# Optimization experiments

Measured on AMD Instinct MI355X. Metric: run time of the kernel, lower is better.

The kernel has to match this reference:

```python
import jax, jax.numpy as jnp
import numpy as np

HIDDEN = 4096
NUM_HEADS = 32
NUM_KV_HEADS = 8
HEAD_DIM = 128
T = 2048
ROPE_THETA = 10000.0


def setup_inputs() -> dict:
    key = jax.random.key(0)
    ks = jax.random.split(key, 10)
    s = 0.02
    return {
        "hidden_states": jax.random.normal(ks[0], (T, HIDDEN), dtype=jnp.float32),
        "positions": jnp.arange(T, dtype=jnp.int32),
        "Wq": jax.random.normal(ks[1], (NUM_HEADS * HEAD_DIM, HIDDEN), dtype=jnp.float32) * s,
        "bq": jax.random.normal(ks[2], (NUM_HEADS * HEAD_DIM,), dtype=jnp.float32) * s,
        "Wk": jax.random.normal(ks[3], (NUM_KV_HEADS * HEAD_DIM, HIDDEN), dtype=jnp.float32) * s,
        "bk": jax.random.normal(ks[4], (NUM_KV_HEADS * HEAD_DIM,), dtype=jnp.float32) * s,
        "Wv": jax.random.normal(ks[5], (NUM_KV_HEADS * HEAD_DIM, HIDDEN), dtype=jnp.float32) * s,
        "bv": jax.random.normal(ks[6], (NUM_KV_HEADS * HEAD_DIM,), dtype=jnp.float32) * s,
        "Wo": jax.random.normal(ks[7], (HIDDEN, HIDDEN), dtype=jnp.float32) * s,
        "bo": jax.random.normal(ks[8], (HIDDEN,), dtype=jnp.float32) * s,
    }


def _rope_cos_sin(positions, head_dim, base):
    # neox-style rotary over the full head_dim
    half = head_dim // 2
    inv_freq = 1.0 / (base ** (jnp.arange(0, half, dtype=jnp.float32) * 2.0 / head_dim))
    angles = positions.astype(jnp.float32)[:, None] * inv_freq[None, :]  # [T, half]
    return jnp.cos(angles), jnp.sin(angles)


def _apply_rope(x, cos, sin):
    # x: [T, H, D]; neox: split halves, rotate
    half = x.shape[-1] // 2
    x1, x2 = x[..., :half], x[..., half:]
    c = cos[:, None, :]
    s = sin[:, None, :]
    return jnp.concatenate([x1 * c - x2 * s, x2 * c + x1 * s], axis=-1)


def reference(hidden_states, positions, Wq, bq, Wk, bk, Wv, bv, Wo, bo):
    q = (hidden_states @ Wq.T + bq).reshape(T, NUM_HEADS, HEAD_DIM)
    k = (hidden_states @ Wk.T + bk).reshape(T, NUM_KV_HEADS, HEAD_DIM)
    v = (hidden_states @ Wv.T + bv).reshape(T, NUM_KV_HEADS, HEAD_DIM)

    cos, sin = _rope_cos_sin(positions, HEAD_DIM, ROPE_THETA)
    q = _apply_rope(q, cos, sin)
    k = _apply_rope(k, cos, sin)

    scale = 1.0 / np.sqrt(HEAD_DIM).astype(np.float32)
    group = NUM_HEADS // NUM_KV_HEADS
    qg = q.reshape(T, NUM_KV_HEADS, group, HEAD_DIM)
    # scores: [g_kv, r, q, k] without materializing repeated KV heads
    scores = jnp.einsum('qgrd,kgd->grqk', qg, k) * scale
    causal = positions[:, None] >= positions[None, :]  # [T, T]
    scores = jnp.where(causal[None, None], scores, jnp.finfo(scores.dtype).min)
    probs = jax.nn.softmax(scores, axis=-1)
    o = jnp.einsum('grqk,kgd->qgrd', probs, v).reshape(T, NUM_HEADS * HEAD_DIM)
    return o @ Wo.T + bo
```

## Files before the change

### kernel.cpp

```cpp
#include <hip/hip_runtime.h>
#include <stdint.h>

typedef unsigned short u16;
typedef __bf16 bf16x8_t __attribute__((ext_vector_type(8)));
typedef float f32x4_t __attribute__((ext_vector_type(4)));

#define T_SEQ 2048
#define HID 4096
#define ROWQKV 6144

__device__ __forceinline__ float bf2f(u16 x){ return __uint_as_float(((uint32_t)x)<<16); }
__device__ __forceinline__ u16 f2bf(float f){
  uint32_t u = __float_as_uint(f);
  return (u16)((u + 0x7fffu + ((u>>16)&1u)) >> 16);
}

__device__ __forceinline__ void gload16(const void* g, void* l){
  __builtin_amdgcn_global_load_lds(
      (const __attribute__((address_space(1))) uint32_t*)g,
      (__attribute__((address_space(3))) uint32_t*)l, 16, 0, 0);
}

__global__ void cvt_kernel(const float* __restrict__ src, u16* __restrict__ dst, int n8){
  int i = blockIdx.x*blockDim.x + threadIdx.x;
  if (i >= n8) return;
  const float4* s = (const float4*)src;
  float4 a = s[2*i], b = s[2*i+1];
  union { u16 u[8]; uint4 v; } o;
  o.u[0]=f2bf(a.x); o.u[1]=f2bf(a.y); o.u[2]=f2bf(a.z); o.u[3]=f2bf(a.w);
  o.u[4]=f2bf(b.x); o.u[5]=f2bf(b.y); o.u[6]=f2bf(b.z); o.u[7]=f2bf(b.w);
  ((uint4*)dst)[i] = o.v;
}

__global__ void setup_kernel(const float* __restrict__ bq, const float* __restrict__ bk,
                             const float* __restrict__ bv, const int* __restrict__ pos,
                             float* __restrict__ bqkv, float* __restrict__ cost,
                             float* __restrict__ sint){
  int i = blockIdx.x*blockDim.x + threadIdx.x;
  if (i < 6144) bqkv[i] = (i<4096) ? bq[i] : ((i<5120) ? bk[i-4096] : bv[i-5120]);
  if (i < T_SEQ*64){
    int t = i >> 6, d = i & 63;
    float inv = powf(10000.0f, -(float)(2*d) / 128.0f);
    float ang = (float)pos[t] * inv;
    cost[i] = cosf(ang);
    sint[i] = sinf(ang);
  }
}

#define BUF2 32768

#define GBAR __builtin_amdgcn_s_barrier()
#define LGKM0 do{ asm volatile("s_waitcnt lgkmcnt(0)" ::: "memory"); \
                  __builtin_amdgcn_sched_barrier(0); }while(0)

#define AREAD2(mh, ck) do{ \
  const u16* ab = &lds[cur + aoff + (mh)*4096]; \
  afr[0] = *(const bf16x8_t*)&ab[0*1024 + (ck)]; \
  afr[1] = *(const bf16x8_t*)&ab[1*1024 + (ck)]; \
  afr[2] = *(const bf16x8_t*)&ab[2*1024 + (ck)]; \
  afr[3] = *(const bf16x8_t*)&ab[3*1024 + (ck)]; }while(0)

#define BREAD2(ck) do{ \
  const u16* bb = &lds[cur + boff]; \
  bfr[0] = *(const bf16x8_t*)&bb[0*1024 + (ck)]; \
  bfr[1] = *(const bf16x8_t*)&bb[1*1024 + (ck)]; \
  bfr[2] = *(const bf16x8_t*)&bb[2*1024 + (ck)]; \
  bfr[3] = *(const bf16x8_t*)&bb[3*1024 + (ck)]; }while(0)

#define MM16(mh) do{ \
  _Pragma("unroll") \
  for (int mi=0; mi<4; ++mi){ \
    _Pragma("unroll") \
    for (int n=0; n<4; ++n) \
      acc[(mh)*4+mi][n] = __builtin_amdgcn_mfma_f32_16x16x32_bf16(afr[mi], bfr[n], acc[(mh)*4+mi][n],0,0,0); \
  } }while(0)

template<bool OUT_BF16>
__global__ __launch_bounds__(512, 2)
void gemm_t2(const u16* __restrict__ A, const u16* __restrict__ B,
             const float* __restrict__ bias, u16* __restrict__ Cb,
             float* __restrict__ Cf, int K, int N)
{
  __shared__ u16 lds[2*BUF2];
  const int tid = threadIdx.x, lane = tid & 63, w = tid >> 6;
  const int l15 = lane & 15, l4 = lane >> 4;
  const int wm = w >> 2, wn = w & 3;

  const int nwg = gridDim.x * gridDim.y;
  int flat = blockIdx.y * gridDim.x + blockIdx.x;
  flat = (flat & 7) * (nwg >> 3) + (flat >> 3);
  const int bx = flat % gridDim.x, by = flat / gridDim.x;
  const int bm = by * 256, bn = bx * 256;

  const int srow = w*8 + (lane >> 3);
  const int swc  = ((lane & 7) ^ (lane >> 3)) * 8;
  const u16* pAlo = A + (size_t)(bm +       srow)*K + swc;
  const u16* pAhi = A + (size_t)(bm + 128 + srow)*K + swc;
  const u16* pBlo = B + (size_t)(bn +       srow)*K + swc;
  const u16* pBhi = B + (size_t)(bn + 128 + srow)*K + swc;
  const size_t j64 = (size_t)64*K;
  const int wu = (w*8)*64;

  const int cA0 = ((0 + l4) ^ (l15 & 7)) * 8;
  const int cA1 = ((4 + l4) ^ (l15 & 7)) * 8;
  const int aoff = (wm*128 + l15) * 64;
  const int boff = 16384 + (wn*64 + l15) * 64;

  f32x4_t acc[8][4] = {};
  const int KT = K >> 6;

  gload16(pAlo,       &lds[0     + wu]);  gload16(pAlo + j64, &lds[4096  + wu]);
  gload16(pAhi,       &lds[8192  + wu]);  gload16(pAhi + j64, &lds[12288 + wu]);
  gload16(pBlo,       &lds[16384 + wu]);  gload16(pBlo + j64, &lds[20480 + wu]);
  gload16(pBhi,       &lds[24576 + wu]);  gload16(pBhi + j64, &lds[28672 + wu]);
  pAlo += 64; pAhi += 64; pBlo += 64; pBhi += 64;
  asm volatile("s_waitcnt vmcnt(0)" ::: "memory");
  GBAR;

  for (int t = 0; t < KT; ++t){
    const int cur = (t & 1) * BUF2;
    const int nxt = ((t + 1) & 1) * BUF2;
    const bool st = (t + 1 < KT);
    bf16x8_t afr[4], bfr[4];

    BREAD2(cA0); AREAD2(0, cA0);
    if (st){
      gload16(pAlo,       &lds[nxt + 0     + wu]);
      gload16(pAlo + j64, &lds[nxt + 4096  + wu]);
      gload16(pAhi,       &lds[nxt + 8192  + wu]);
      gload16(pAhi + j64, &lds[nxt + 12288 + wu]);
    }
    GBAR; LGKM0;
    __builtin_amdgcn_s_setprio(1); MM16(0); __builtin_amdgcn_s_setprio(0);
    GBAR;

    AREAD2(1, cA0);
    if (st){
      gload16(pBlo,       &lds[nxt + 16384 + wu]);
      gload16(pBlo + j64, &lds[nxt + 20480 + wu]);
      gload16(pBhi,       &lds[nxt + 24576 + wu]);
      gload16(pBhi + j64, &lds[nxt + 28672 + wu]);
      pAlo += 64; pAhi += 64; pBlo += 64; pBhi += 64;
    }
    GBAR; LGKM0;
    __builtin_amdgcn_s_setprio(1); MM16(1); __builtin_amdgcn_s_setprio(0);
    GBAR;

    BREAD2(cA1); AREAD2(0, cA1);
    GBAR; LGKM0;
    __builtin_amdgcn_s_setprio(1); MM16(0); __builtin_amdgcn_s_setprio(0);
    GBAR;

    AREAD2(1, cA1);
    GBAR; LGKM0;
    __builtin_amdgcn_s_setprio(1); MM16(1); __builtin_amdgcn_s_setprio(0);
    if (st) asm volatile("s_waitcnt vmcnt(0)" ::: "memory");
    GBAR;
  }

  #pragma unroll
  for (int m=0;m<8;m++){
    #pragma unroll
    for (int n=0;n<4;n++){
      #pragma unroll
      for (int j=0;j<4;j++){
        int row = bm + wm*128 + (m>>2)*64 + (m&3)*16 + l4*4 + j;
        int col = bn + wn*64 + n*16 + l15;
        float v = acc[m][n][j] + bias[col];
        if constexpr (OUT_BF16) Cb[(size_t)row*N + col] = f2bf(v);
        else                    Cf[(size_t)row*N + col] = v;
      }
    }
  }
}

__global__ void rope_kernel(u16* __restrict__ qkv, const float* __restrict__ cost,
                            const float* __restrict__ sint){
  int i = blockIdx.x*blockDim.x + threadIdx.x;
  int t = i / 2560;
  int r = i % 2560;
  int h = r >> 6, d = r & 63;
  int base = (h < 32) ? h*128 : (4096 + (h-32)*128);
  size_t p1 = (size_t)t*ROWQKV + base + d;
  float x1 = bf2f(qkv[p1]), x2 = bf2f(qkv[p1+64]);
  float c = cost[(t<<6)+d], s = sint[(t<<6)+d];
  qkv[p1]    = f2bf(x1*c - x2*s);
  qkv[p1+64] = f2bf(x2*c + x1*s);
}

#define KLD 136
#define VLD 72
#define PLD 72

__global__ __launch_bounds__(256)
void attn_kernel(const u16* __restrict__ qkv, u16* __restrict__ attn_o)
{
  __shared__ u16 Ks[64*KLD];
  __shared__ u16 Vt[128*VLD];
  __shared__ u16 Ps[64*PLD];
  const int tid = threadIdx.x, lane = tid&63, wid = tid>>6;
  const int l15 = lane&15, l4 = lane>>4;
  const int h  = blockIdx.x & 31;
  const int qt = 31 - (blockIdx.x >> 5);
  const int q0 = qt * 64;
  const int kvh = h >> 2;
  const u16* Qg = qkv + h*128;
  const u16* Kg = qkv + 4096 + kvh*128;
  const u16* Vg = qkv + 5120 + kvh*128;

  bf16x8_t qf[4];
  {
    size_t qrow = (size_t)(q0 + wid*16 + l15);
    #pragma unroll
    for (int kk=0;kk<4;kk++)
      qf[kk] = *(const bf16x8_t*)(Qg + qrow*ROWQKV + kk*32 + l4*8);
  }
  float mrow[4] = {-1e30f,-1e30f,-1e30f,-1e30f};
  float lrow[4] = {0.f,0.f,0.f,0.f};
  f32x4_t oacc[8] = {};
  const float scale = 0.08838834764831845f;

  const int krow = tid >> 2, kd0 = (tid & 3) * 32;
  const int kvp  = tid & 31;
  const int vd0  = (tid >> 5) * 16;

  for (int kt = 0; kt <= qt; ++kt){
    int kv0 = kt * 64;
    {
      const u16* src = Kg + (size_t)(kv0 + krow)*ROWQKV + kd0;
      #pragma unroll
      for (int i=0;i<4;i++)
        *(uint4*)&Ks[krow*KLD + kd0 + i*8] = *(const uint4*)(src + i*8);
      const u16* va = Vg + (size_t)(kv0 + 2*kvp)*ROWQKV + vd0;
      uint4 r0 = *(const uint4*)va,            r1 = *(const uint4*)(va + 8);
      uint4 r2 = *(const uint4*)(va + ROWQKV), r3 = *(const uint4*)(va + ROWQKV + 8);
      const u16* ra = (const u16*)&r0; const u16* rb = (const u16*)&r2;
      #pragma unroll
      for (int e=0;e<8;e++)
        *(uint32_t*)&Vt[(vd0 + e)*VLD + 2*kvp] = (uint32_t)ra[e] | ((uint32_t)rb[e] << 16);
      ra = (const u16*)&r1; rb = (const u16*)&r3;
      #pragma unroll
      for (int e=0;e<8;e++)
        *(uint32_t*)&Vt[(vd0 + 8 + e)*VLD + 2*kvp] = (uint32_t)ra[e] | ((uint32_t)rb[e] << 16);
    }
    __syncthreads();

    f32x4_t sacc[4] = {};
    #pragma unroll
    for (int n=0;n<4;n++){
      #pragma unroll
      for (int kk=0;kk<4;kk++){
        bf16x8_t kf = *(const bf16x8_t*)&Ks[(n*16 + l15)*KLD + kk*32 + l4*8];
        sacc[n] = __builtin_amdgcn_mfma_f32_16x16x32_bf16(qf[kk], kf, sacc[n], 0,0,0);
      }
    }
    float sv[4][4];
    float pmax[4] = {-1e30f,-1e30f,-1e30f,-1e30f};
    bool diag = (kt == qt);
    #pragma unroll
    for (int n=0;n<4;n++){
      int kvcol = kv0 + n*16 + l15;
      #pragma unroll
      for (int j=0;j<4;j++){
        float s = sacc[n][j] * scale;
        int qrow = q0 + wid*16 + l4*4 + j;
        if (diag && kvcol > qrow) s = -1e30f;
        sv[n][j] = s;
        pmax[j] = fmaxf(pmax[j], s);
      }
    }
    #pragma unroll
    for (int off=1; off<16; off<<=1){
      #pragma unroll
      for (int j=0;j<4;j++)
        pmax[j] = fmaxf(pmax[j], __shfl_xor(pmax[j], off, 64));
    }
    float esc[4], rsum[4] = {0.f,0.f,0.f,0.f};
    #pragma unroll
    for (int j=0;j<4;j++){
      float mn = fmaxf(mrow[j], pmax[j]);
      esc[j] = __expf(mrow[j] - mn);
      mrow[j] = mn;
    }
    #pragma unroll
    for (int n=0;n<4;n++){
      #pragma unroll
      for (int j=0;j<4;j++){
        float p = __expf(sv[n][j] - mrow[j]);
        sv[n][j] = p;
        rsum[j] += p;
      }
    }
    #pragma unroll
    for (int off=1; off<16; off<<=1){
      #pragma unroll
      for (int j=0;j<4;j++)
        rsum[j] += __shfl_xor(rsum[j], off, 64);
    }
    #pragma unroll
    for (int j=0;j<4;j++) lrow[j] = lrow[j]*esc[j] + rsum[j];
    #pragma unroll
    for (int n=0;n<8;n++){
      #pragma unroll
      for (int j=0;j<4;j++) oacc[n][j] *= esc[j];
    }
    #pragma unroll
    for (int n=0;n<4;n++){
      #pragma unroll
      for (int j=0;j<4;j++)
        Ps[(wid*16 + l4*4 + j)*PLD + n*16 + l15] = f2bf(sv[n][j]);
    }
    #pragma unroll
    for (int kk=0;kk<2;kk++){
      bf16x8_t pf = *(const bf16x8_t*)&Ps[(wid*16 + l15)*PLD + kk*32 + l4*8];
      #pragma unroll
      for (int n=0;n<8;n++){
        bf16x8_t vf = *(const bf16x8_t*)&Vt[(n*16 + l15)*VLD + kk*32 + l4*8];
        oacc[n] = __builtin_amdgcn_mfma_f32_16x16x32_bf16(pf, vf, oacc[n], 0,0,0);
      }
    }
    __syncthreads();
  }

  #pragma unroll
  for (int n=0;n<8;n++){
    #pragma unroll
    for (int j=0;j<4;j++){
      int qrow = q0 + wid*16 + l4*4 + j;
      int col  = h*128 + n*16 + l15;
      attn_o[(size_t)qrow*HID + col] = f2bf(oacc[n][j] / lrow[j]);
    }
  }
}

extern "C" void kernel_launch(void* const* d_in, const int* in_sizes, int n_in,
                              void* d_out, int out_size, void* d_ws, size_t ws_size,
                              hipStream_t stream)
{
  const float* hs = (const float*)d_in[0];
  const int*  pos = (const int*)d_in[1];
  const float* Wq = (const float*)d_in[2];
  const float* bq = (const float*)d_in[3];
  const float* Wk = (const float*)d_in[4];
  const float* bk = (const float*)d_in[5];
  const float* Wv = (const float*)d_in[6];
  const float* bv = (const float*)d_in[7];
  const float* Wo = (const float*)d_in[8];
  const float* bo = (const float*)d_in[9];
  float* out = (float*)d_out;

  char* ws = (char*)d_ws;
  u16* hs_bf   = (u16*)ws;  ws += (size_t)2048*4096*2;
  u16* Wqkv_bf = (u16*)ws;  ws += (size_t)6144*4096*2;
  u16* Wo_bf   = (u16*)ws;  ws += (size_t)4096*4096*2;
  u16* qkv     = (u16*)ws;  ws += (size_t)2048*6144*2;
  u16* attn_b  = (u16*)ws;  ws += (size_t)2048*4096*2;
  float* bqkv  = (float*)ws; ws += (size_t)6144*4;
  float* cost  = (float*)ws; ws += (size_t)2048*64*4;
  float* sint  = (float*)ws; ws += (size_t)2048*64*4;

  {
    int n8 = 2048*4096/8;
    cvt_kernel<<<(n8+255)/256, 256, 0, stream>>>(hs, hs_bf, n8);
    n8 = 4096*4096/8;
    cvt_kernel<<<(n8+255)/256, 256, 0, stream>>>(Wq, Wqkv_bf, n8);
    n8 = 1024*4096/8;
    cvt_kernel<<<(n8+255)/256, 256, 0, stream>>>(Wk, Wqkv_bf + (size_t)4096*4096, n8);
    cvt_kernel<<<(n8+255)/256, 256, 0, stream>>>(Wv, Wqkv_bf + (size_t)5120*4096, n8);
    n8 = 4096*4096/8;
    cvt_kernel<<<(n8+255)/256, 256, 0, stream>>>(Wo, Wo_bf, n8);
  }
  setup_kernel<<<(T_SEQ*64 + 255)/256, 256, 0, stream>>>(bq, bk, bv, pos, bqkv, cost, sint);

  gemm_t2<true><<<dim3(6144/256, 2048/256), 512, 0, stream>>>(hs_bf, Wqkv_bf, bqkv, qkv, nullptr, 4096, 6144);
  rope_kernel<<<(T_SEQ*40*64)/256, 256, 0, stream>>>(qkv, cost, sint);
  attn_kernel<<<1024, 256, 0, stream>>>(qkv, attn_b);
  gemm_t2<false><<<dim3(4096/256, 2048/256), 512, 0, stream>>>(attn_b, Wo_bf, bo, nullptr, out, 4096, 4096);
}
```

Measured before the change: 398.3 us.

## Double-buffer K via async global-to-LDS loads and prefetch V with XOR-swizzled LDS

The attention kernel now prefetches the next K tile straight into a second LDS buffer with global_load_lds. It also loads the next V tile into registers while the current tile's MFMAs run, then transposes V into LDS after a barrier. Padded LDS strides are replaced by XOR-swizzled 64-wide layouts for K, V and P to avoid bank conflicts without wasting space. The aim is to hide global load latency and cut LDS conflicts, at the cost of an extra barrier per iteration and more registers for the V prefetch.

```diff
diff --git a/kernel.cpp b/kernel.cpp
--- a/kernel.cpp
+++ b/kernel.cpp
@@ -188,18 +188,16 @@
   qkv[p1+64] = f2bf(x2*c + x1*s);
 }
 
-#define KLD 136
-#define VLD 72
-#define PLD 72
+#define VOFF 16384
+#define POFF 24576
 
 __global__ __launch_bounds__(256)
 void attn_kernel(const u16* __restrict__ qkv, u16* __restrict__ attn_o)
 {
-  __shared__ u16 Ks[64*KLD];
-  __shared__ u16 Vt[128*VLD];
-  __shared__ u16 Ps[64*PLD];
+  __shared__ u16 lds[28672];
   const int tid = threadIdx.x, lane = tid&63, wid = tid>>6;
   const int l15 = lane&15, l4 = lane>>4;
+  const int l7 = l15 & 7;
   const int h  = blockIdx.x & 31;
   const int qt = 31 - (blockIdx.x >> 5);
   const int q0 = qt * 64;
@@ -220,37 +218,65 @@
   f32x4_t oacc[8] = {};
   const float scale = 0.08838834764831845f;
 
-  const int krow = tid >> 2, kd0 = (tid & 3) * 32;
-  const int kvp  = tid & 31;
-  const int vd0  = (tid >> 5) * 16;
+  const u16* ksrc[4];
+  int kls[4];
+  #pragma unroll
+  for (int i=0;i<4;i++){
+    const int c = wid*4 + i;
+    ksrc[i] = Kg + (size_t)((c&7)*8 + (lane>>3))*ROWQKV
+               + (c>>3)*64 + ((lane&7)^(lane>>3))*8;
+    kls[i] = c*512;
+  }
+  const int kvp = tid & 31;
+  const int vd0 = (tid >> 5) * 16;
+  uint4 rv[4];
+
+  #pragma unroll
+  for (int i=0;i<4;i++) gload16(ksrc[i], &lds[kls[i]]);
+  #pragma unroll
+  for (int i=0;i<4;i++) ksrc[i] += (size_t)64*ROWQKV;
+  {
+    const u16* va = Vg + (size_t)(2*kvp)*ROWQKV + vd0;
+    rv[0] = *(const uint4*)va;            rv[1] = *(const uint4*)(va + 8);
+    rv[2] = *(const uint4*)(va + ROWQKV); rv[3] = *(const uint4*)(va + ROWQKV + 8);
+  }
+  __syncthreads();
+  {
+    const u16* ra = (const u16*)&rv[0]; const u16* rb = (const u16*)&rv[2];
+    #pragma unroll
+    for (int e=0;e<8;e++)
+      *(uint32_t*)&lds[VOFF + (vd0+e)*64 + ((kvp>>2)^(e&7))*8 + 2*(kvp&3)]
+          = (uint32_t)ra[e] | ((uint32_t)rb[e] << 16);
+    ra = (const u16*)&rv[1]; rb = (const u16*)&rv[3];
+    #pragma unroll
+    for (int e=0;e<8;e++)
+      *(uint32_t*)&lds[VOFF + (vd0+8+e)*64 + ((kvp>>2)^(e&7))*8 + 2*(kvp&3)]
+          = (uint32_t)ra[e] | ((uint32_t)rb[e] << 16);
+  }
+  __syncthreads();
 
   for (int kt = 0; kt <= qt; ++kt){
-    int kv0 = kt * 64;
-    {
-      const u16* src = Kg + (size_t)(kv0 + krow)*ROWQKV + kd0;
-      #pragma unroll
-      for (int i=0;i<4;i++)
-        *(uint4*)&Ks[krow*KLD + kd0 + i*8] = *(const uint4*)(src + i*8);
-      const u16* va = Vg + (size_t)(kv0 + 2*kvp)*ROWQKV + vd0;
-      uint4 r0 = *(const uint4*)va,            r1 = *(const uint4*)(va + 8);
-      uint4 r2 = *(const uint4*)(va + ROWQKV), r3 = *(const uint4*)(va + ROWQKV + 8);
-      const u16* ra = (const u16*)&r0; const u16* rb = (const u16*)&r2;
-      #pragma unroll
-      for (int e=0;e<8;e++)
-        *(uint32_t*)&Vt[(vd0 + e)*VLD + 2*kvp] = (uint32_t)ra[e] | ((uint32_t)rb[e] << 16);
-      ra = (const u16*)&r1; rb = (const u16*)&r3;
-      #pragma unroll
-      for (int e=0;e<8;e++)
-        *(uint32_t*)&Vt[(vd0 + 8 + e)*VLD + 2*kvp] = (uint32_t)ra[e] | ((uint32_t)rb[e] << 16);
-    }
-    __syncthreads();
+    const int kv0 = kt * 64;
+    const int kcur = (kt & 1) * 8192;
+    const bool pre = (kt < qt);
+    if (pre){
+      const int knxt = ((kt+1) & 1) * 8192;
+      #pragma unroll
+      for (int i=0;i<4;i++) gload16(ksrc[i], &lds[knxt + kls[i]]);
+      #pragma unroll
+      for (int i=0;i<4;i++) ksrc[i] += (size_t)64*ROWQKV;
+      const u16* va = Vg + (size_t)(kv0 + 64 + 2*kvp)*ROWQKV + vd0;
+      rv[0] = *(const uint4*)va;            rv[1] = *(const uint4*)(va + 8);
+      rv[2] = *(const uint4*)(va + ROWQKV); rv[3] = *(const uint4*)(va + ROWQKV + 8);
+    }
 
     f32x4_t sacc[4] = {};
     #pragma unroll
     for (int n=0;n<4;n++){
       #pragma unroll
       for (int kk=0;kk<4;kk++){
-        bf16x8_t kf = *(const bf16x8_t*)&Ks[(n*16 + l15)*KLD + kk*32 + l4*8];
+        bf16x8_t kf = *(const bf16x8_t*)&lds[kcur + (kk>>1)*4096
+                        + (n*16+l15)*64 + (((kk&1)*4 + l4) ^ l7)*8];
         sacc[n] = __builtin_amdgcn_mfma_f32_16x16x32_bf16(qf[kk], kf, sacc[n], 0,0,0);
       }
     }
@@ -308,16 +334,31 @@
     for (int n=0;n<4;n++){
       #pragma unroll
       for (int j=0;j<4;j++)
-        Ps[(wid*16 + l4*4 + j)*PLD + n*16 + l15] = f2bf(sv[n][j]);
+        lds[POFF + (wid*16 + l4*4 + j)*64
+            + (((n*2 + (l15>>3)) ^ ((l4*4+j)&7))*8) + l7] = f2bf(sv[n][j]);
     }
     #pragma unroll
     for (int kk=0;kk<2;kk++){
-      bf16x8_t pf = *(const bf16x8_t*)&Ps[(wid*16 + l15)*PLD + kk*32 + l4*8];
+      const int blk = ((kk*4 + l4) ^ l7)*8;
+      bf16x8_t pf = *(const bf16x8_t*)&lds[POFF + (wid*16 + l15)*64 + blk];
       #pragma unroll
       for (int n=0;n<8;n++){
-        bf16x8_t vf = *(const bf16x8_t*)&Vt[(n*16 + l15)*VLD + kk*32 + l4*8];
+        bf16x8_t vf = *(const bf16x8_t*)&lds[VOFF + (n*16 + l15)*64 + blk];
         oacc[n] = __builtin_amdgcn_mfma_f32_16x16x32_bf16(pf, vf, oacc[n], 0,0,0);
       }
+    }
+    __syncthreads();
+    if (pre){
+      const u16* ra = (const u16*)&rv[0]; const u16* rb = (const u16*)&rv[2];
+      #pragma unroll
+      for (int e=0;e<8;e++)
+        *(uint32_t*)&lds[VOFF + (vd0+e)*64 + ((kvp>>2)^(e&7))*8 + 2*(kvp&3)]
+            = (uint32_t)ra[e] | ((uint32_t)rb[e] << 16);
+      ra = (const u16*)&rv[1]; rb = (const u16*)&rv[3];
+      #pragma unroll
+      for (int e=0;e<8;e++)
+        *(uint32_t*)&lds[VOFF + (vd0+8+e)*64 + ((kvp>>2)^(e&7))*8 + 2*(kvp&3)]
+            = (uint32_t)ra[e] | ((uint32_t)rb[e] << 16);
     }
     __syncthreads();
   }
```

New measurement: 394.3 us. No clear change (-1.0%).
